# Optimization experiments

Measured on AMD Instinct MI355X. Metric: run time of the kernel, lower is better.

Reference implementation:

```python
import jax, jax.numpy as jnp
import numpy as np

HEADS = 8
DIM_HEAD = 64
LN_EPS = 1e-5


def _layernorm(x, gamma, beta):
    mu = jnp.mean(x, axis=-1, keepdims=True)
    var = jnp.var(x, axis=-1, keepdims=True)
    return (x - mu) * jax.lax.rsqrt(var + LN_EPS) * gamma + beta


def setup_inputs() -> dict:
    key = jax.random.key(0)
    ks = jax.random.split(key, 5)
    B, N, D = 1, 16384, 512
    return {
        "x": jax.random.normal(ks[0], (B, N, D), dtype=jnp.float32),
        "ln_gamma": jnp.ones((D,), dtype=jnp.float32),
        "ln_beta": jnp.zeros((D,), dtype=jnp.float32),
        "w_qkv": jax.random.normal(ks[1], (D, 3 * D), dtype=jnp.float32) * (D ** -0.5),
        "agent": jax.random.normal(ks[2], (HEADS, 512, DIM_HEAD), dtype=jnp.float32) * (DIM_HEAD ** -0.5),
        "w_out": jax.random.normal(ks[3], (D, D), dtype=jnp.float32) * (D ** -0.5),
        "b_out": jnp.zeros((D,), dtype=jnp.float32),
    }


def reference(x, ln_gamma, ln_beta, w_qkv, agent, w_out, b_out):
    # TransLayer: x + Mask_Agent_Attention(LayerNorm(x))
    B, N, D = x.shape
    xn = _layernorm(x, ln_gamma, ln_beta)

    qkv = xn @ w_qkv                                   # [B, N, 3D]
    q, k, v = jnp.split(qkv, 3, axis=-1)
    # [B, H, N, d]
    q = q.reshape(B, N, HEADS, DIM_HEAD).transpose(0, 2, 1, 3)
    k = k.reshape(B, N, HEADS, DIM_HEAD).transpose(0, 2, 1, 3)
    v = v.reshape(B, N, HEADS, DIM_HEAD).transpose(0, 2, 1, 3)

    scale = DIM_HEAD ** -0.5  # tem=0 -> classical 1/sqrt(d) scaling

    # agents aggregate values: softmax over keys  [B, H, A, N]
    attn1 = jax.nn.softmax(jnp.einsum('had,bhnd->bhan', agent, k) * scale, axis=-1)
    agent_v = jnp.einsum('bhan,bhnd->bhad', attn1, v)  # [B, H, A, d]

    # queries attend to agents: softmax over agents  [B, H, N, A]
    attn2 = jax.nn.softmax(jnp.einsum('bhnd,had->bhna', q, agent) * scale, axis=-1)
    out = jnp.einsum('bhna,bhad->bhnd', attn2, agent_v)  # [B, H, N, d]

    out = out + v  # residual=True: value residual inside attention
    out = out.transpose(0, 2, 1, 3).reshape(B, N, D)
    out = out @ w_out + b_out
    return x + out
```

## Files before the change

kernel.cpp:

```cpp
#include <hip/hip_runtime.h>
#include <stdint.h>

typedef unsigned short u16;
typedef __attribute__((ext_vector_type(8))) short bf16x8;
typedef __attribute__((ext_vector_type(4))) float f32x4;

__device__ __forceinline__ float bf2f(u16 u){
  union { uint32_t i; float f; } v; v.i = ((uint32_t)u) << 16; return v.f;
}
__device__ __forceinline__ u16 f2bf(float f){
  union { float fl; uint32_t i; } v; v.fl = f;
  uint32_t r = v.i + 0x7FFFu + ((v.i >> 16) & 1u);
  return (u16)(r >> 16);
}
__device__ __forceinline__ uint32_t cvt_pk_bf16(float lo, float hi){
  uint32_t r;
  asm("v_cvt_pk_bf16_f32 %0, %1, %2" : "=v"(r) : "v"(lo), "v"(hi));
  return r;
}
__device__ __forceinline__ f32x4 mfma16(bf16x8 a, bf16x8 b, f32x4 c){
  return __builtin_amdgcn_mfma_f32_16x16x32_bf16(a, b, c, 0, 0, 0);
}
__device__ __forceinline__ void gload16(const u16* g, u16* l){
  __builtin_amdgcn_global_load_lds((const __attribute__((address_space(1))) void*)g,
                                   (__attribute__((address_space(3))) void*)l, 16, 0, 0);
}

__global__ __launch_bounds__(256) void k_conv_bf(const float* __restrict__ in, u16* __restrict__ out, int n, float scale){
  int i = (blockIdx.x * 256 + threadIdx.x) * 4;
  if (i >= n) return;
  float4 v = *(const float4*)(in + i);
  ushort4 o; o.x=f2bf(v.x*scale); o.y=f2bf(v.y*scale); o.z=f2bf(v.z*scale); o.w=f2bf(v.w*scale);
  *(ushort4*)(out + i) = o;
}

__global__ __launch_bounds__(256) void k_transp(const float* __restrict__ in, u16* __restrict__ out, int R, int C){
  __shared__ u16 tile[64][68];
  int c0 = blockIdx.x * 64, r0 = blockIdx.y * 64;
  int tr = threadIdx.x >> 4;
  int tc = (threadIdx.x & 15) * 4;
  for (int rr = 0; rr < 4; rr++){
    int r = rr * 16 + tr;
    float4 v = *(const float4*)(in + (size_t)(r0 + r) * C + c0 + tc);
    ushort4 o; o.x=f2bf(v.x); o.y=f2bf(v.y); o.z=f2bf(v.z); o.w=f2bf(v.w);
    *(ushort4*)&tile[r][tc] = o;
  }
  __syncthreads();
  for (int rr = 0; rr < 4; rr++){
    int oc = rr * 16 + tr;
    ushort4 o;
    o.x = tile[tc+0][oc]; o.y = tile[tc+1][oc]; o.z = tile[tc+2][oc]; o.w = tile[tc+3][oc];
    *(ushort4*)(out + (size_t)(c0 + oc) * R + r0 + tc) = o;
  }
}

__global__ __launch_bounds__(128) void k_ln(const float* __restrict__ x, const float* __restrict__ g,
                                            const float* __restrict__ b, u16* __restrict__ xn){
  int row = blockIdx.x;
  int t = threadIdx.x;
  float4 v = *(const float4*)(x + (size_t)row * 512 + t * 4);
  float s = v.x + v.y + v.z + v.w;
  float q = v.x*v.x + v.y*v.y + v.z*v.z + v.w*v.w;
  for (int o = 32; o > 0; o >>= 1){ s += __shfl_down(s, o); q += __shfl_down(q, o); }
  __shared__ float red[4];
  if ((t & 63) == 0){ red[(t >> 6) * 2] = s; red[(t >> 6) * 2 + 1] = q; }
  __syncthreads();
  float mu  = (red[0] + red[2]) * (1.0f/512.0f);
  float var = (red[1] + red[3]) * (1.0f/512.0f) - mu * mu;
  float rs = rsqrtf(var + 1e-5f);
  float4 gv = *(const float4*)(g + t * 4);
  float4 bv = *(const float4*)(b + t * 4);
  ushort4 o;
  o.x = f2bf((v.x - mu) * rs * gv.x + bv.x);
  o.y = f2bf((v.y - mu) * rs * gv.y + bv.y);
  o.z = f2bf((v.z - mu) * rs * gv.z + bv.z);
  o.w = f2bf((v.w - mu) * rs * gv.w + bv.w);
  *(ushort4*)(xn + (size_t)row * 512 + t * 4) = o;
}


__global__ __launch_bounds__(512) void k_gemm_qkv(const u16* __restrict__ A, const u16* __restrict__ Bt,
                                                  u16* __restrict__ C, u16* __restrict__ vT){
  __shared__ u16 aL[2][256 * 64];
  __shared__ u16 bL[2][128 * 64];
  int m0 = blockIdx.x * 256, n0 = blockIdx.y * 128;
  int t = threadIdx.x, w = t >> 6, l = t & 63;
  int wm = (w >> 1) * 64, wn = (w & 1) * 64;
  int lr = l & 15;
  int blkSrc = (l & 7) ^ ((l >> 3) & 7);
  const u16* gA = A  + (size_t)(m0 + w*8 + (l >> 3)) * 512 + blkSrc * 8;
  const u16* gB = Bt + (size_t)(n0 + w*8 + (l >> 3)) * 512 + blkSrc * 8;
  f32x4 acc[4][4];
  for (int i=0;i<4;i++) for (int j=0;j<4;j++) acc[i][j] = {0.f,0.f,0.f,0.f};

  auto stage = [&](int buf, int k0){
    #pragma unroll
    for (int p = 0; p < 4; p++)
      gload16(gA + (size_t)p*64*512 + k0, &aL[buf][(p*64 + w*8) * 64]);
    #pragma unroll
    for (int p = 0; p < 2; p++)
      gload16(gB + (size_t)p*64*512 + k0, &bL[buf][(p*64 + w*8) * 64]);
  };
  auto comp = [&](const u16* ab, const u16* bb){
    #pragma unroll
    for (int kk = 0; kk < 64; kk += 32){
      int xo = (((l >> 4) + (kk >> 3)) ^ (l & 7)) << 3;
      bf16x8 av[4], bv[4];
      #pragma unroll
      for (int mt=0;mt<4;mt++) av[mt] = *(const bf16x8*)&ab[(wm + mt*16 + lr)*64 + xo];
      #pragma unroll
      for (int nt=0;nt<4;nt++) bv[nt] = *(const bf16x8*)&bb[(wn + nt*16 + lr)*64 + xo];
      #pragma unroll
      for (int mt=0;mt<4;mt++)
        #pragma unroll
        for (int nt=0;nt<4;nt++)
          acc[mt][nt] = mfma16(av[mt], bv[nt], acc[mt][nt]);
    }
  };

  stage(0, 0);
  stage(1, 64);
  asm volatile("s_waitcnt vmcnt(6)" ::: "memory");
  __builtin_amdgcn_s_barrier();
  asm volatile("" ::: "memory");
  int cur = 0;
  #pragma unroll
  for (int tk = 0; tk < 8; tk++){
    comp(&aL[cur][0], &bL[cur][0]);
    if (tk < 7){
      __builtin_amdgcn_s_barrier();
      if (tk + 2 < 8){
        stage(cur, (tk + 2) * 64);
        asm volatile("s_waitcnt vmcnt(6)" ::: "memory");
      } else {
        asm volatile("s_waitcnt vmcnt(0)" ::: "memory");
      }
      __builtin_amdgcn_s_barrier();
      asm volatile("" ::: "memory");
    }
    cur ^= 1;
  }

  int rr = (l >> 4) * 4, cc = l & 15;
  bool isV = (n0 >= 1024);
  for (int mt=0;mt<4;mt++) for (int nt=0;nt<4;nt++){
    int r = m0 + wm + mt*16 + rr;
    int c = n0 + wn + nt*16 + cc;
    ushort4 o;
    o.x = f2bf(acc[mt][nt][0]); o.y = f2bf(acc[mt][nt][1]);
    o.z = f2bf(acc[mt][nt][2]); o.w = f2bf(acc[mt][nt][3]);
    C[(size_t)(r+0) * 1536 + c] = o.x;
    C[(size_t)(r+1) * 1536 + c] = o.y;
    C[(size_t)(r+2) * 1536 + c] = o.z;
    C[(size_t)(r+3) * 1536 + c] = o.w;
    if (isV) *(ushort4*)(vT + ((size_t)(c - 1024) << 14) + r) = o;
  }
}

__global__ __launch_bounds__(512) void k_gemm_out(const u16* __restrict__ A, const u16* __restrict__ Bt,
                                                  const float* __restrict__ x, const float* __restrict__ bias,
                                                  float* __restrict__ y){
  __shared__ u16 aL[2][256 * 64];
  __shared__ u16 bL[2][128 * 64];
  int m0 = blockIdx.x * 256, n0 = blockIdx.y * 128;
  int t = threadIdx.x, w = t >> 6, l = t & 63;
  int wm = (w >> 1) * 64, wn = (w & 1) * 64;
  int lr = l & 15;
  int blkSrc = (l & 7) ^ ((l >> 3) & 7);
  const u16* gA = A  + (size_t)(m0 + w*8 + (l >> 3)) * 512 + blkSrc * 8;
  const u16* gB = Bt + (size_t)(n0 + w*8 + (l >> 3)) * 512 + blkSrc * 8;
  f32x4 acc[4][4];
  for (int i=0;i<4;i++) for (int j=0;j<4;j++) acc[i][j] = {0.f,0.f,0.f,0.f};

  auto stage = [&](int buf, int k0){
    #pragma unroll
    for (int p = 0; p < 4; p++)
      gload16(gA + (size_t)p*64*512 + k0, &aL[buf][(p*64 + w*8) * 64]);
    #pragma unroll
    for (int p = 0; p < 2; p++)
      gload16(gB + (size_t)p*64*512 + k0, &bL[buf][(p*64 + w*8) * 64]);
  };
  auto comp = [&](const u16* ab, const u16* bb){
    #pragma unroll
    for (int kk = 0; kk < 64; kk += 32){
      int xo = (((l >> 4) + (kk >> 3)) ^ (l & 7)) << 3;
      bf16x8 av[4], bv[4];
      #pragma unroll
      for (int mt=0;mt<4;mt++) av[mt] = *(const bf16x8*)&ab[(wm + mt*16 + lr)*64 + xo];
      #pragma unroll
      for (int nt=0;nt<4;nt++) bv[nt] = *(const bf16x8*)&bb[(wn + nt*16 + lr)*64 + xo];
      #pragma unroll
      for (int mt=0;mt<4;mt++)
        #pragma unroll
        for (int nt=0;nt<4;nt++)
          acc[mt][nt] = mfma16(av[mt], bv[nt], acc[mt][nt]);
    }
  };

  stage(0, 0);
  stage(1, 64);
  asm volatile("s_waitcnt vmcnt(6)" ::: "memory");
  __builtin_amdgcn_s_barrier();
  asm volatile("" ::: "memory");
  int cur = 0;
  #pragma unroll
  for (int tk = 0; tk < 8; tk++){
    comp(&aL[cur][0], &bL[cur][0]);
    if (tk < 7){
      __builtin_amdgcn_s_barrier();
      if (tk + 2 < 8){
        stage(cur, (tk + 2) * 64);
        asm volatile("s_waitcnt vmcnt(6)" ::: "memory");
      } else {
        asm volatile("s_waitcnt vmcnt(0)" ::: "memory");
      }
      __builtin_amdgcn_s_barrier();
      asm volatile("" ::: "memory");
    }
    cur ^= 1;
  }

  int rr = (l >> 4) * 4, cc = l & 15;
  for (int mt=0;mt<4;mt++) for (int nt=0;nt<4;nt++)
    for (int j=0;j<4;j++){
      int r = m0 + wm + mt*16 + rr + j;
      int c = n0 + wn + nt*16 + cc;
      y[(size_t)r * 512 + c] = acc[mt][nt][j] + bias[c] + x[(size_t)r * 512 + c];
    }
}

__global__ __launch_bounds__(256) void k_agent_agg(const u16* __restrict__ agbf, const u16* __restrict__ qkv,
                                                   const u16* __restrict__ vT,
                                                   float* __restrict__ nump, float* __restrict__ denp){
  int L = blockIdx.x;
  int g = (L >> 6) * 8 + (L & 7);
  int m = (L >> 3) & 7;
  int h = g >> 4, ch = g & 15, a0 = m * 64;

  __shared__ u16 ag[64][72];
  __shared__ u16 kt[64][72];
  __shared__ u16 vt[64][72];
  __shared__ u16 pt[64][72];
  int t = threadIdx.x, w = t >> 6, l = t & 63;

  for (int i = 0; i < 2; i++){
    int flat = t + 256 * i;
    int r = flat >> 3, c = (flat & 7) * 8;
    *(uint4*)&ag[r][c] = *(const uint4*)(agbf + (size_t)(h * 512 + a0 + r) * 64 + c);
  }

  bf16x8 ones;
  for (int i = 0; i < 8; i++) ones[i] = (short)0x3F80;

  f32x4 acc2[4];
  for (int i=0;i<4;i++) acc2[i] = {0.f,0.f,0.f,0.f};
  f32x4 accd = {0.f,0.f,0.f,0.f};

  for (int sub = 0; sub < 16; sub++){
    int n0 = ch * 1024 + sub * 64;
    __syncthreads();
    {
      int flat = t;
      int r = flat >> 3, c = (flat & 7) * 8;
      *(uint4*)&kt[r][c] = *(const uint4*)(qkv + (size_t)(n0 + r) * 1536 + 512 + h * 64 + c);
      int flat2 = t + 256;
      int r2 = flat2 >> 3, c2 = (flat2 & 7) * 8;
      *(uint4*)&kt[r2][c2] = *(const uint4*)(qkv + (size_t)(n0 + r2) * 1536 + 512 + h * 64 + c2);
      *(uint4*)&vt[r][c]   = *(const uint4*)(vT + ((size_t)(h * 64 + r) << 14) + n0 + c);
      *(uint4*)&vt[r2][c2] = *(const uint4*)(vT + ((size_t)(h * 64 + r2) << 14) + n0 + c2);
    }
    __syncthreads();

    f32x4 s[4];
    for (int nt=0;nt<4;nt++) s[nt] = {0.f,0.f,0.f,0.f};
    for (int kk = 0; kk < 64; kk += 32){
      int kb = kk + (l >> 4) * 8;
      bf16x8 kf = *(const bf16x8*)&kt[w*16 + (l & 15)][kb];
      for (int nt=0;nt<4;nt++){
        bf16x8 af = *(const bf16x8*)&ag[nt*16 + (l & 15)][kb];
        s[nt] = mfma16(kf, af, s[nt]);
      }
    }
    int nb = w*16 + (l >> 4) * 4;
    for (int nt=0;nt<4;nt++){
      int a = nt*16 + (l & 15);
      uint32_t w0 = cvt_pk_bf16(__builtin_amdgcn_exp2f(s[nt][0]), __builtin_amdgcn_exp2f(s[nt][1]));
      uint32_t w1 = cvt_pk_bf16(__builtin_amdgcn_exp2f(s[nt][2]), __builtin_amdgcn_exp2f(s[nt][3]));
      uint2 o; o.x = w0; o.y = w1;
      *(uint2*)&pt[a][nb] = o;
    }
    __syncthreads();

    for (int kk = 0; kk < 64; kk += 32){
      int kb = kk + (l >> 4) * 8;
      bf16x8 vf = *(const bf16x8*)&vt[w*16 + (l & 15)][kb];
      for (int mt=0;mt<4;mt++){
        bf16x8 pf = *(const bf16x8*)&pt[mt*16 + (l & 15)][kb];
        acc2[mt] = mfma16(pf, vf, acc2[mt]);
      }
      bf16x8 pw = *(const bf16x8*)&pt[w*16 + (l & 15)][kb];
      accd = mfma16(ones, pw, accd);
    }
  }

  size_t base = ((size_t)(h * 16 + ch) * 512 + a0) * 64;
  for (int mt=0;mt<4;mt++)
    #pragma unroll
    for (int j=0;j<4;j++){
      int a = mt*16 + (l>>4)*4 + j;
      int d = w*16 + (l&15);
      nump[base + (size_t)a*64 + d] = acc2[mt][j];
    }
  if (l < 16) denp[(size_t)(h*16 + ch) * 512 + a0 + w*16 + l] = accd[0];
}

__global__ __launch_bounds__(64) void k_agent_reduce(const float* __restrict__ nump, const float* __restrict__ denp,
                                                     u16* __restrict__ avtg){
  int h = blockIdx.x >> 9;
  int a = blockIdx.x & 511;
  int d = threadIdx.x;
  float num = 0.f, den = 0.f;
  for (int c = 0; c < 16; c++){
    num += nump[((size_t)(h * 16 + c) * 512 + a) * 64 + d];
    den += denp[(size_t)(h * 16 + c) * 512 + a];
  }
  avtg[((size_t)h * 64 + d) * 512 + a] = f2bf(num / den);
}

__global__ __launch_bounds__(256) void k_qattn(const u16* __restrict__ qkv, const u16* __restrict__ agbf,
                                               const u16* __restrict__ avtg, u16* __restrict__ atto){
  int n0 = blockIdx.x * 64;
  int h  = blockIdx.y;
  __shared__ u16 agL[2][64][68];
  __shared__ u16 avL[2][64][68];
  __shared__ u16 pt[2][64][68];
  __shared__ float dnf[4][64];
  int t = threadIdx.x, w = t >> 6, l = t & 63;
  int lr = l & 15, q4 = l >> 4;

  bf16x8 qf[4][2];
  #pragma unroll
  for (int nt=0;nt<4;nt++)
    #pragma unroll
    for (int kk=0;kk<2;kk++)
      qf[nt][kk] = *(const bf16x8*)(qkv + (size_t)(n0 + nt*16 + lr) * 1536 + h*64 + kk*32 + q4*8);

  int sr = t >> 2, sc = (t & 3) * 16;
  uint4 rg0, rg1, rv0, rv1;
  rg0 = *(const uint4*)(agbf + (size_t)(h*512 + sr) * 64 + sc);
  rg1 = *(const uint4*)(agbf + (size_t)(h*512 + sr) * 64 + sc + 8);
  rv0 = *(const uint4*)(avtg + (size_t)(h*64 + sr) * 512 + sc);
  rv1 = *(const uint4*)(avtg + (size_t)(h*64 + sr) * 512 + sc + 8);
  *(uint4*)&agL[0][sr][sc]     = rg0;
  *(uint4*)&agL[0][sr][sc + 8] = rg1;
  *(uint4*)&avL[0][sr][sc]     = rv0;
  *(uint4*)&avL[0][sr][sc + 8] = rv1;
  __syncthreads();

  f32x4 acc[4];
  #pragma unroll
  for (int i=0;i<4;i++) acc[i] = {0.f,0.f,0.f,0.f};
  float den[4] = {0.f,0.f,0.f,0.f};

  for (int at = 0; at < 8; at++){
    int cur = at & 1, prv = cur ^ 1;
    if (at + 1 < 8){
      rg0 = *(const uint4*)(agbf + (size_t)(h*512 + (at+1)*64 + sr) * 64 + sc);
      rg1 = *(const uint4*)(agbf + (size_t)(h*512 + (at+1)*64 + sr) * 64 + sc + 8);
      rv0 = *(const uint4*)(avtg + (size_t)(h*64 + sr) * 512 + (at+1)*64 + sc);
      rv1 = *(const uint4*)(avtg + (size_t)(h*64 + sr) * 512 + (at+1)*64 + sc + 8);
    }
    f32x4 s[4];
    #pragma unroll
    for (int nt=0;nt<4;nt++) s[nt] = {0.f,0.f,0.f,0.f};
    #pragma unroll
    for (int kk = 0; kk < 2; kk++){
      bf16x8 af = *(const bf16x8*)&agL[cur][w*16 + lr][kk*32 + q4*8];
      #pragma unroll
      for (int nt=0;nt<4;nt++)
        s[nt] = mfma16(af, qf[nt][kk], s[nt]);
    }
    #pragma unroll
    for (int nt=0;nt<4;nt++){
      float e0 = __builtin_amdgcn_exp2f(s[nt][0]);
      float e1 = __builtin_amdgcn_exp2f(s[nt][1]);
      float e2 = __builtin_amdgcn_exp2f(s[nt][2]);
      float e3 = __builtin_amdgcn_exp2f(s[nt][3]);
      den[nt] += (e0 + e1) + (e2 + e3);
      uint2 o; o.x = cvt_pk_bf16(e0, e1); o.y = cvt_pk_bf16(e2, e3);
      *(uint2*)&pt[cur][nt*16 + lr][w*16 + q4*4] = o;
    }
    if (at > 0){
      #pragma unroll
      for (int kk = 0; kk < 64; kk += 32){
        int kb = kk + q4*8;
        bf16x8 vf = *(const bf16x8*)&avL[prv][w*16 + lr][kb];
        #pragma unroll
        for (int mt=0;mt<4;mt++){
          bf16x8 pf = *(const bf16x8*)&pt[prv][mt*16 + lr][kb];
          acc[mt] = mfma16(pf, vf, acc[mt]);
        }
      }
    }
    __syncthreads();
    if (at + 1 < 8){
      *(uint4*)&agL[prv][sr][sc]     = rg0;
      *(uint4*)&agL[prv][sr][sc + 8] = rg1;
      *(uint4*)&avL[prv][sr][sc]     = rv0;
      *(uint4*)&avL[prv][sr][sc + 8] = rv1;
    }
    __syncthreads();
  }
  {
    #pragma unroll
    for (int kk = 0; kk < 64; kk += 32){
      int kb = kk + q4*8;
      bf16x8 vf = *(const bf16x8*)&avL[1][w*16 + lr][kb];
      #pragma unroll
      for (int mt=0;mt<4;mt++){
        bf16x8 pf = *(const bf16x8*)&pt[1][mt*16 + lr][kb];
        acc[mt] = mfma16(pf, vf, acc[mt]);
      }
    }
  }

  float dq[4];
  #pragma unroll
  for (int nt=0;nt<4;nt++){
    float r = den[nt];
    r += __shfl_xor(r, 16);
    r += __shfl_xor(r, 32);
    dq[nt] = r;
  }
  if (q4 == 0)
    #pragma unroll
    for (int nt=0;nt<4;nt++) dnf[w][nt*16 + lr] = dq[nt];
  __syncthreads();
  if (t < 64){
    float sden = dnf[0][t] + dnf[1][t] + dnf[2][t] + dnf[3][t];
    dnf[0][t] = __builtin_amdgcn_rcpf(sden);
  }
  __syncthreads();

  int d = w*16 + lr;
  #pragma unroll
  for (int mt=0;mt<4;mt++){
    #pragma unroll
    for (int j=0;j<4;j++){
      int n = mt*16 + q4*4 + j;
      float v = bf2f(qkv[(size_t)(n0 + n) * 1536 + 1024 + h * 64 + d]);
      atto[(size_t)(n0 + n) * 512 + h * 64 + d] = f2bf(acc[mt][j] * dnf[0][n] + v);
    }
  }
}

extern "C" void kernel_launch(void* const* d_in, const int* in_sizes, int n_in,
                              void* d_out, int out_size, void* d_ws, size_t ws_size,
                              hipStream_t stream) {
  const float* x     = (const float*)d_in[0];
  const float* gamma = (const float*)d_in[1];
  const float* beta  = (const float*)d_in[2];
  const float* w_qkv = (const float*)d_in[3];
  const float* agent = (const float*)d_in[4];
  const float* w_out = (const float*)d_in[5];
  const float* b_out = (const float*)d_in[6];
  float* y = (float*)d_out;

  char* ws = (char*)d_ws;
  u16*   xn    = (u16*)  (ws + 0);
  u16*   qkv   = (u16*)  (ws + 16777216);
  u16*   wqkvt = (u16*)  (ws + 67108864);
  u16*   woutt = (u16*)  (ws + 68681728);
  u16*   agbf  = (u16*)  (ws + 69206016);
  u16*   avtg  = (u16*)  (ws + 69730304);
  u16*   vT    = (u16*)  (ws + 70254592);
  u16*   atto  = (u16*)  (ws + 70254592);
  float* nump  = (float*)(ws + 87031808);
  float* denp  = (float*)(ws + 103809024);

  k_conv_bf   <<<dim3(256),     dim3(256), 0, stream>>>(agent, agbf, 8*512*64, 0.125f * 1.44269504089f);
  k_transp    <<<dim3(24, 8),   dim3(256), 0, stream>>>(w_qkv, wqkvt, 512, 1536);
  k_transp    <<<dim3(8, 8),    dim3(256), 0, stream>>>(w_out, woutt, 512, 512);
  k_ln        <<<dim3(16384),   dim3(128), 0, stream>>>(x, gamma, beta, xn);
  k_gemm_qkv  <<<dim3(64, 12),  dim3(512), 0, stream>>>(xn, wqkvt, qkv, vT);
  k_agent_agg <<<dim3(1024),    dim3(256), 0, stream>>>(agbf, qkv, vT, nump, denp);
  k_agent_reduce<<<dim3(4096),  dim3(64),  0, stream>>>(nump, denp, avtg);
  k_qattn     <<<dim3(256, 8),  dim3(256), 0, stream>>>(qkv, agbf, avtg, atto);
  k_gemm_out  <<<dim3(64, 4),   dim3(512), 0, stream>>>(atto, woutt, x, b_out, y);
}
```

Before: 155.7 us.

## Software-pipeline agent aggregation with double-buffered K/V/P tiles and register prefetch

Restructures the k_agent_agg loop so the next K/V tile is prefetched into registers and written to a second LDS buffer, while the P·V product for the previous tile runs alongside the current score computation. This cuts the per-iteration barriers from three to two and overlaps global loads with MFMA work. The denominator now comes from fp32 exp sums reduced with shuffles instead of a ones-vector MFMA, and the LDS row padding changes from 72 to 68. LDS use rises from the double buffers, and the new padding may alter bank-conflict behaviour.

New measurement: 157.2 us. About the same (+1.0%).

```diff
diff --git a/kernel.cpp b/kernel.cpp
--- a/kernel.cpp
+++ b/kernel.cpp
@@ -77,7 +77,6 @@
   o.w = f2bf((v.w - mu) * rs * gv.w + bv.w);
   *(ushort4*)(xn + (size_t)row * 512 + t * 4) = o;
 }
-
 
 __global__ __launch_bounds__(512) void k_gemm_qkv(const u16* __restrict__ A, const u16* __restrict__ Bt,
                                                   u16* __restrict__ C, u16* __restrict__ vT){
@@ -237,11 +236,13 @@
   int m = (L >> 3) & 7;
   int h = g >> 4, ch = g & 15, a0 = m * 64;
 
-  __shared__ u16 ag[64][72];
-  __shared__ u16 kt[64][72];
-  __shared__ u16 vt[64][72];
-  __shared__ u16 pt[64][72];
+  __shared__ u16 ag[64][68];
+  __shared__ u16 ktL[2][64][68];
+  __shared__ u16 vtL[2][64][68];
+  __shared__ u16 ptL[2][64][68];
+  __shared__ float dnf[4][64];
   int t = threadIdx.x, w = t >> 6, l = t & 63;
+  int lr = l & 15, q4 = l >> 4;
 
   for (int i = 0; i < 2; i++){
     int flat = t + 256 * i;
@@ -249,69 +250,112 @@
     *(uint4*)&ag[r][c] = *(const uint4*)(agbf + (size_t)(h * 512 + a0 + r) * 64 + c);
   }
 
-  bf16x8 ones;
-  for (int i = 0; i < 8; i++) ones[i] = (short)0x3F80;
+  int sr = t >> 2, sc = (t & 3) * 16;
+  size_t nbase = (size_t)ch * 1024;
+  const u16* kp = qkv + 512 + h * 64;
+  const u16* vp = vT + ((size_t)(h * 64 + sr) << 14);
+  uint4 rk0, rk1, rv0, rv1;
+  rk0 = *(const uint4*)(kp + (nbase + sr) * 1536 + sc);
+  rk1 = *(const uint4*)(kp + (nbase + sr) * 1536 + sc + 8);
+  rv0 = *(const uint4*)(vp + nbase + sc);
+  rv1 = *(const uint4*)(vp + nbase + sc + 8);
+  *(uint4*)&ktL[0][sr][sc]     = rk0;
+  *(uint4*)&ktL[0][sr][sc + 8] = rk1;
+  *(uint4*)&vtL[0][sr][sc]     = rv0;
+  *(uint4*)&vtL[0][sr][sc + 8] = rv1;
+  __syncthreads();
 
   f32x4 acc2[4];
+  #pragma unroll
   for (int i=0;i<4;i++) acc2[i] = {0.f,0.f,0.f,0.f};
-  f32x4 accd = {0.f,0.f,0.f,0.f};
+  float den[4] = {0.f,0.f,0.f,0.f};
 
   for (int sub = 0; sub < 16; sub++){
-    int n0 = ch * 1024 + sub * 64;
+    int cur = sub & 1, prv = cur ^ 1;
+    if (sub + 1 < 16){
+      size_t n1 = nbase + (sub + 1) * 64;
+      rk0 = *(const uint4*)(kp + (n1 + sr) * 1536 + sc);
+      rk1 = *(const uint4*)(kp + (n1 + sr) * 1536 + sc + 8);
+      rv0 = *(const uint4*)(vp + n1 + sc);
+      rv1 = *(const uint4*)(vp + n1 + sc + 8);
+    }
+    f32x4 s[4];
+    #pragma unroll
+    for (int nt=0;nt<4;nt++) s[nt] = {0.f,0.f,0.f,0.f};
+    #pragma unroll
+    for (int kk = 0; kk < 64; kk += 32){
+      int kb = kk + q4 * 8;
+      bf16x8 kf = *(const bf16x8*)&ktL[cur][w*16 + lr][kb];
+      #pragma unroll
+      for (int nt=0;nt<4;nt++){
+        bf16x8 af = *(const bf16x8*)&ag[nt*16 + lr][kb];
+        s[nt] = mfma16(kf, af, s[nt]);
+      }
+    }
+    #pragma unroll
+    for (int nt=0;nt<4;nt++){
+      float e0 = __builtin_amdgcn_exp2f(s[nt][0]);
+      float e1 = __builtin_amdgcn_exp2f(s[nt][1]);
+      float e2 = __builtin_amdgcn_exp2f(s[nt][2]);
+      float e3 = __builtin_amdgcn_exp2f(s[nt][3]);
+      den[nt] += (e0 + e1) + (e2 + e3);
+      uint2 o; o.x = cvt_pk_bf16(e0, e1); o.y = cvt_pk_bf16(e2, e3);
+      *(uint2*)&ptL[cur][nt*16 + lr][w*16 + q4*4] = o;
+    }
+    if (sub > 0){
+      #pragma unroll
+      for (int kk = 0; kk < 64; kk += 32){
+        int kb = kk + q4 * 8;
+        bf16x8 vf = *(const bf16x8*)&vtL[prv][w*16 + lr][kb];
+        #pragma unroll
+        for (int mt=0;mt<4;mt++){
+          bf16x8 pf = *(const bf16x8*)&ptL[prv][mt*16 + lr][kb];
+          acc2[mt] = mfma16(pf, vf, acc2[mt]);
+        }
+      }
+    }
     __syncthreads();
-    {
-      int flat = t;
-      int r = flat >> 3, c = (flat & 7) * 8;
-      *(uint4*)&kt[r][c] = *(const uint4*)(qkv + (size_t)(n0 + r) * 1536 + 512 + h * 64 + c);
-      int flat2 = t + 256;
-      int r2 = flat2 >> 3, c2 = (flat2 & 7) * 8;
-      *(uint4*)&kt[r2][c2] = *(const uint4*)(qkv + (size_t)(n0 + r2) * 1536 + 512 + h * 64 + c2);
-      *(uint4*)&vt[r][c]   = *(const uint4*)(vT + ((size_t)(h * 64 + r) << 14) + n0 + c);
-      *(uint4*)&vt[r2][c2] = *(const uint4*)(vT + ((size_t)(h * 64 + r2) << 14) + n0 + c2);
+    if (sub + 1 < 16){
+      *(uint4*)&ktL[prv][sr][sc]     = rk0;
+      *(uint4*)&ktL[prv][sr][sc + 8] = rk1;
+      *(uint4*)&vtL[prv][sr][sc]     = rv0;
+      *(uint4*)&vtL[prv][sr][sc + 8] = rv1;
     }
     __syncthreads();
-
-    f32x4 s[4];
-    for (int nt=0;nt<4;nt++) s[nt] = {0.f,0.f,0.f,0.f};
+  }
+  {
+    #pragma unroll
     for (int kk = 0; kk < 64; kk += 32){
-      int kb = kk + (l >> 4) * 8;
-      bf16x8 kf = *(const bf16x8*)&kt[w*16 + (l & 15)][kb];
-      for (int nt=0;nt<4;nt++){
-        bf16x8 af = *(const bf16x8*)&ag[nt*16 + (l & 15)][kb];
-        s[nt] = mfma16(kf, af, s[nt]);
-      }
-    }
-    int nb = w*16 + (l >> 4) * 4;
-    for (int nt=0;nt<4;nt++){
-      int a = nt*16 + (l & 15);
-      uint32_t w0 = cvt_pk_bf16(__builtin_amdgcn_exp2f(s[nt][0]), __builtin_amdgcn_exp2f(s[nt][1]));
-      uint32_t w1 = cvt_pk_bf16(__builtin_amdgcn_exp2f(s[nt][2]), __builtin_amdgcn_exp2f(s[nt][3]));
-      uint2 o; o.x = w0; o.y = w1;
-      *(uint2*)&pt[a][nb] = o;
-    }
-    __syncthreads();
-
-    for (int kk = 0; kk < 64; kk += 32){
-      int kb = kk + (l >> 4) * 8;
-      bf16x8 vf = *(const bf16x8*)&vt[w*16 + (l & 15)][kb];
+      int kb = kk + q4 * 8;
+      bf16x8 vf = *(const bf16x8*)&vtL[1][w*16 + lr][kb];
+      #pragma unroll
       for (int mt=0;mt<4;mt++){
-        bf16x8 pf = *(const bf16x8*)&pt[mt*16 + (l & 15)][kb];
+        bf16x8 pf = *(const bf16x8*)&ptL[1][mt*16 + lr][kb];
         acc2[mt] = mfma16(pf, vf, acc2[mt]);
       }
-      bf16x8 pw = *(const bf16x8*)&pt[w*16 + (l & 15)][kb];
-      accd = mfma16(ones, pw, accd);
-    }
-  }
+    }
+  }
+
+  #pragma unroll
+  for (int nt=0;nt<4;nt++){
+    float r = den[nt];
+    r += __shfl_xor(r, 16);
+    r += __shfl_xor(r, 32);
+    if (q4 == 0) dnf[w][nt*16 + lr] = r;
+  }
+  __syncthreads();
 
   size_t base = ((size_t)(h * 16 + ch) * 512 + a0) * 64;
+  #pragma unroll
   for (int mt=0;mt<4;mt++)
     #pragma unroll
     for (int j=0;j<4;j++){
-      int a = mt*16 + (l>>4)*4 + j;
-      int d = w*16 + (l&15);
+      int a = mt*16 + q4*4 + j;
+      int d = w*16 + lr;
       nump[base + (size_t)a*64 + d] = acc2[mt][j];
     }
-  if (l < 16) denp[(size_t)(h*16 + ch) * 512 + a0 + w*16 + l] = accd[0];
+  if (t < 64)
+    denp[(size_t)(h*16 + ch) * 512 + a0 + t] = dnf[0][t] + dnf[1][t] + dnf[2][t] + dnf[3][t];
 }
 
 __global__ __launch_bounds__(64) void k_agent_reduce(const float* __restrict__ nump, const float* __restrict__ denp,
```
